# Optimization experiments

Hardware: AMD Instinct MI355X
Metric: run time of the kernel (lower is better)

## Reference

```python
import jax, jax.numpy as jnp
import numpy as np

DIM, HID, NC = 512, 102, 64
B, NS, ND, M = 256, 196, 196, 40
EPS_LN = 1e-5


def setup_inputs() -> dict:
    key = jax.random.key(0)
    ks = jax.random.split(key, 8)
    s = lambda d: 1.0 / np.sqrt(d)
    return {
        "tokens_sparse": jax.random.normal(ks[0], (B, NS, DIM), jnp.float32),
        "tokens_dense": jax.random.normal(ks[1], (B, ND, DIM), jnp.float32),
        "words": jax.random.normal(ks[2], (B, M, DIM), jnp.float32),
        "ln_g_s": jnp.ones((DIM,), jnp.float32),
        "ln_b_s": jnp.zeros((DIM,), jnp.float32),
        "w1_s": jax.random.normal(ks[3], (DIM, HID), jnp.float32) * s(DIM),
        "b1_s": jnp.zeros((HID,), jnp.float32),
        "w2_s": jax.random.normal(ks[4], (HID, NC), jnp.float32) * s(HID),
        "b2_s": jnp.zeros((NC,), jnp.float32),
        "ln_g_d": jnp.ones((DIM,), jnp.float32),
        "ln_b_d": jnp.zeros((DIM,), jnp.float32),
        "w1_d": jax.random.normal(ks[5], (DIM, HID), jnp.float32) * s(DIM),
        "b1_d": jnp.zeros((HID,), jnp.float32),
        "w2_d": jax.random.normal(ks[6], (HID, NC), jnp.float32) * s(HID),
        "b2_d": jnp.zeros((NC,), jnp.float32),
        "scale": jnp.ones((1, 1, 1), jnp.float32),
    }


def _layernorm(x, g, b):
    mu = x.mean(-1, keepdims=True)
    var = ((x - mu) ** 2).mean(-1, keepdims=True)
    return (x - mu) * jax.lax.rsqrt(var + EPS_LN) * g + b


def _aggregate(x, ln_g, ln_b, w1, b1, w2, b2, scale):
    # weight = MLP(LN(x)) -> (B, N, NC); transpose -> (B, NC, N); softmax over N; bmm
    h = jax.nn.gelu(_layernorm(x, ln_g, ln_b) @ w1 + b1, approximate=False)
    w = jnp.swapaxes(h @ w2 + b2, 1, 2) * scale            # (B, NC, N)
    w = jax.nn.softmax(w, axis=2)
    return jnp.einsum("bkn,bnc->bkc", w, x)                 # (B, NC, C)


def _l2norm(x):
    return x / jnp.maximum(jnp.linalg.norm(x, axis=-1, keepdims=True), 1e-8)


def reference(tokens_sparse, tokens_dense, words,
              ln_g_s, ln_b_s, w1_s, b1_s, w2_s, b2_s,
              ln_g_d, ln_b_d, w1_d, b1_d, w2_d, b2_d, scale):
    # DualTokenAggregation: paper Eq.(4)
    agg = _aggregate(tokens_sparse, ln_g_s, ln_b_s, w1_s, b1_s, w2_s, b2_s, scale)
    agg = agg + _aggregate(tokens_dense, ln_g_d, ln_b_d, w1_d, b1_d, w2_d, b2_d, scale)
    v = _l2norm(agg)                                        # (B, NC, C)
    t = _l2norm(words)                                      # (B, M, C)
    # HRPA (scan=True, bidirectional, no mask): bmm + leaky_relu + max/mean pooling
    sim = jnp.einsum("bmc,bkc->bmk", t, v)                  # (B, M, NC)
    sim = jnp.where(sim >= 0, sim, 0.1 * sim)               # leaky_relu(0.1)
    row_mean = sim.max(axis=2).mean(axis=1, keepdims=True)  # word->patch
    col_mean = sim.max(axis=1).mean(axis=1, keepdims=True)  # patch->word
    return row_mean + col_mean                              # (B, 1)
```

## Files before the change

### kernel.cpp

```cpp
#include <hip/hip_runtime.h>
#include <hip/hip_fp16.h>
#include <math.h>

#define Bb 256
#define Nn 196
#define Dd 512
#define Hh 102
#define Kk 64
#define Mm 40

#define LOGITS_BYTES 25690112
#define W1H_OFF  ((size_t)25690112)
#define W1L_OFF  (W1H_OFF + 262144)
#define GWB1_OFF (W1L_OFF + 262144)
#define W2TH_OFF (GWB1_OFF + 2048)
#define W2TL_OFF (W2TH_OFF + 32768)
#define H_OFF    (W2TL_OFF + 32768)
#define HL_OFF   (H_OFF + 29360128)
#define AGG_OFF  (HL_OFF + 29360128)

using short8 = __attribute__((ext_vector_type(8))) short;
using f32x4  = __attribute__((ext_vector_type(4))) float;

__device__ __forceinline__ void barrier_lgkm_only() {
  asm volatile("s_waitcnt lgkmcnt(0)" ::: "memory");
  __builtin_amdgcn_s_barrier();
  asm volatile("" ::: "memory");
}

__device__ __forceinline__ float dot4(const float4 a, const float4 b) {
  return a.x*b.x + a.y*b.y + a.z*b.z + a.w*b.w;
}
__device__ __forceinline__ float4 ld4s(const float* p) { return *(const float4*)p; }
__device__ __forceinline__ float gelu1(float z) {
  return 0.5f * z * (1.f + erff(z * 0.70710678118f));
}
__device__ __forceinline__ unsigned short bf16hi(float v) {
  return (unsigned short)(__float_as_uint(v) >> 16);
}
__device__ __forceinline__ float hipart(float v) {
  return __uint_as_float(__float_as_uint(v) & 0xffff0000u);
}
__device__ __forceinline__ unsigned short f2h(float v) {
  __half h = __float2half(v);
  return *(unsigned short*)&h;
}
__device__ __forceinline__ float h2f(unsigned short u) {
  __half h = *(__half*)&u;
  return __half2float(h);
}
__device__ __forceinline__ void split8(const float4 va, const float4 vb,
                                       short8& hh, short8& ll) {
  hh[0] = (short)bf16hi(va.x); ll[0] = (short)bf16hi(va.x - hipart(va.x));
  hh[1] = (short)bf16hi(va.y); ll[1] = (short)bf16hi(va.y - hipart(va.y));
  hh[2] = (short)bf16hi(va.z); ll[2] = (short)bf16hi(va.z - hipart(va.z));
  hh[3] = (short)bf16hi(va.w); ll[3] = (short)bf16hi(va.w - hipart(va.w));
  hh[4] = (short)bf16hi(vb.x); ll[4] = (short)bf16hi(vb.x - hipart(vb.x));
  hh[5] = (short)bf16hi(vb.y); ll[5] = (short)bf16hi(vb.y - hipart(vb.y));
  hh[6] = (short)bf16hi(vb.z); ll[6] = (short)bf16hi(vb.z - hipart(vb.z));
  hh[7] = (short)bf16hi(vb.w); ll[7] = (short)bf16hi(vb.w - hipart(vb.w));
}
__device__ __forceinline__ float wave_reduce_sum(float v) {
#pragma unroll
  for (int o = 1; o < 64; o <<= 1) v += __shfl_xor(v, o, 64);
  return v;
}
__device__ __forceinline__ float wave_reduce_max(float v) {
#pragma unroll
  for (int o = 1; o < 64; o <<= 1) v = fmaxf(v, __shfl_xor(v, o, 64));
  return v;
}

__global__ __launch_bounds__(512) void k0_wprep(
    const float* __restrict__ g_s, const float* __restrict__ b_s,
    const float* __restrict__ w1_s, const float* __restrict__ b1_s,
    const float* __restrict__ w2_s,
    const float* __restrict__ g_d, const float* __restrict__ b_d,
    const float* __restrict__ w1_d, const float* __restrict__ b1_d,
    const float* __restrict__ w2_d,
    unsigned short* __restrict__ w1h, unsigned short* __restrict__ w1l,
    float* __restrict__ gwb1,
    unsigned short* __restrict__ w2th, unsigned short* __restrict__ w2tl)
{
  const int p = blockIdx.x, slice = blockIdx.y;
  const float* g  = p ? g_d  : g_s;
  const float* bb = p ? b_d  : b_s;
  const float* w1 = p ? w1_d : w1_s;
  const float* b1 = p ? b1_d : b1_s;
  const float* w2 = p ? w2_d : w2_s;
  const int tid = threadIdx.x;

  if (slice < 8) {
    for (int idx = slice * 8192 + tid; idx < slice * 8192 + 8192; idx += 512) {
      const int j = idx & 127, c = idx >> 7;
      const float v = (j < Hh) ? w1[(size_t)c * Hh + j] * g[c] : 0.f;
      w1h[((size_t)(p * 128 + j)) * 512 + c] = bf16hi(v);
      w1l[((size_t)(p * 128 + j)) * 512 + c] = bf16hi(v - hipart(v));
    }
  } else {
    for (int idx = tid; idx < 8192; idx += 512) {
      const int k = idx >> 7, j = idx & 127;
      const float v = (j < Hh) ? w2[(size_t)j * Kk + k] : 0.f;
      w2th[(size_t)(p * 64 + k) * 128 + j] = bf16hi(v);
      w2tl[(size_t)(p * 64 + k) * 128 + j] = bf16hi(v - hipart(v));
    }
  }

  if (slice == 0) {
    __shared__ float red[4][128][2];
    const int j = tid & 127, part = tid >> 7;
    float sg = 0.f, sb = 0.f;
    if (j < Hh) {
      for (int c = part * 128; c < part * 128 + 128; ++c) {
        const float w = w1[(size_t)c * Hh + j];
        sg += g[c] * w;
        sb += bb[c] * w;
      }
    }
    red[part][j][0] = sg;
    red[part][j][1] = sb;
    __syncthreads();
    if (part == 0) {
      const float G  = red[0][j][0] + red[1][j][0] + red[2][j][0] + red[3][j][0];
      const float Bv = red[0][j][1] + red[1][j][1] + red[2][j][1] + red[3][j][1];
      gwb1[(p * 128 + j) * 2]     = G;
      gwb1[(p * 128 + j) * 2 + 1] = (j < Hh) ? (Bv + b1[j]) : 0.f;
    }
  }
}

__global__ __launch_bounds__(512) void k1a_hgemm(
    const float* __restrict__ x_s, const float* __restrict__ x_d,
    const unsigned short* __restrict__ w1h, const unsigned short* __restrict__ w1l,
    const float* __restrict__ gwb1,
    unsigned short* __restrict__ h_hi, unsigned short* __restrict__ h_lo)
{
  __shared__ __align__(16) char smem1[40320];
  unsigned short* xbuf = (unsigned short*)smem1;
  float* part = (float*)(smem1 + 35840);
  float* st   = (float*)(smem1 + 39424);

  const int tid = threadIdx.x;
  const int ntile = blockIdx.x, p = blockIdx.y, b = blockIdx.z;
  const int nbase = ntile * 112;
  const float* x  = p ? x_d : x_s;

  const int lane = tid & 63, wv = tid >> 6;
  const int lr = lane & 15, lg = lane >> 4;
  const int jb = wv * 16;
  const unsigned short* wph = w1h + ((size_t)(p * 128 + jb + lr)) * 512 + lg * 8;
  const unsigned short* wpl = w1l + ((size_t)(p * 128 + jb + lr)) * 512 + lg * 8;

  const int t = tid >> 2, q = tid & 3;
  const bool stg = (tid < 448);
  const int n = nbase + t;
  const bool valid = stg && (n < Nn);
  const float* xrow = x + ((size_t)(b * Nn + (valid ? n : 0))) * Dd + q * 8;

  float psum = 0.f, psq = 0.f;
  f32x4 acc0 = {0,0,0,0}, acc1 = acc0, acc2 = acc0, acc3 = acc0;
  f32x4 acc4 = acc0, acc5 = acc0, acc6 = acc0;

  short8 bh_c = *(const short8*)(wph);
  short8 bl_c = *(const short8*)(wpl);

  {
    float4 va = {0,0,0,0}, vb = va;
    if (valid) { va = ld4s(xrow); vb = ld4s(xrow + 4); }
    if (stg) {
      psum += va.x + va.y + va.z + va.w + vb.x + vb.y + vb.z + vb.w;
      psq  += dot4(va, va) + dot4(vb, vb);
      short8 hh, ll;
      split8(va, vb, hh, ll);
      *(short8*)(xbuf + t * 40 + q * 8) = hh;
      *(short8*)(xbuf + 4480 + t * 40 + q * 8) = ll;
    }
  }
  float4 pva = {0,0,0,0}, pvb = pva;
  if (valid) { pva = ld4s(xrow + 32); pvb = ld4s(xrow + 36); }
  barrier_lgkm_only();

#pragma unroll 1
  for (int ch = 0; ch < 16; ++ch) {
    const int buf = ch & 1;
    const unsigned short* xh = xbuf + buf * 8960;
    const unsigned short* xl = xh + 4480;

    float4 nva = {0,0,0,0}, nvb = nva;
    if (ch < 14 && valid) {
      const int co = (ch + 2) * 32;
      nva = ld4s(xrow + co);
      nvb = ld4s(xrow + co + 4);
    }
    short8 bh_n = bh_c, bl_n = bl_c;
    if (ch < 15) {
      const int co = (ch + 1) * 32;
      bh_n = *(const short8*)(wph + co);
      bl_n = *(const short8*)(wpl + co);
    }

#define MSTEP(A, M) { \
    const short8 ah = *(const short8*)(xh + ((M) * 16 + lr) * 40 + lg * 8); \
    const short8 al = *(const short8*)(xl + ((M) * 16 + lr) * 40 + lg * 8); \
    (A) = __builtin_amdgcn_mfma_f32_16x16x32_bf16(ah, bh_c, (A), 0, 0, 0); \
    (A) = __builtin_amdgcn_mfma_f32_16x16x32_bf16(ah, bl_c, (A), 0, 0, 0); \
    (A) = __builtin_amdgcn_mfma_f32_16x16x32_bf16(al, bh_c, (A), 0, 0, 0); }
    MSTEP(acc0, 0) MSTEP(acc1, 1) MSTEP(acc2, 2) MSTEP(acc3, 3)
    MSTEP(acc4, 4) MSTEP(acc5, 5) MSTEP(acc6, 6)
#undef MSTEP

    if (ch < 15 && stg) {
      psum += pva.x + pva.y + pva.z + pva.w + pvb.x + pvb.y + pvb.z + pvb.w;
      psq  += dot4(pva, pva) + dot4(pvb, pvb);
      short8 hh, ll;
      split8(pva, pvb, hh, ll);
      unsigned short* xw = xbuf + (buf ^ 1) * 8960;
      *(short8*)(xw + t * 40 + q * 8) = hh;
      *(short8*)(xw + 4480 + t * 40 + q * 8) = ll;
    }
    pva = nva; pvb = nvb;
    bh_c = bh_n; bl_c = bl_n;
    barrier_lgkm_only();
  }

  if (stg) {
    part[t * 8 + q * 2]     = psum;
    part[t * 8 + q * 2 + 1] = psq;
  }
  __syncthreads();
  if (tid < 112) {
    const float s  = part[tid * 8] + part[tid * 8 + 2] + part[tid * 8 + 4] + part[tid * 8 + 6];
    const float ss = part[tid * 8 + 1] + part[tid * 8 + 3] + part[tid * 8 + 5] + part[tid * 8 + 7];
    const float mu  = s * (1.f / 512.f);
    const float var = fmaxf(ss * (1.f / 512.f) - mu * mu, 0.f);
    st[2 * tid]     = mu;
    st[2 * tid + 1] = rsqrtf(var + 1e-5f);
  }
  __syncthreads();

  const int colw = jb + lr;
  const float Gw = gwb1[(p * 128 + colw) * 2];
  const float B1 = gwb1[(p * 128 + colw) * 2 + 1];
  const size_t hoff = (size_t)((b * 2 + p) * 2 + ntile) * 14336 + colw;
#define HW1(A, M) { \
    _Pragma("unroll") \
    for (int rr = 0; rr < 4; ++rr) { \
      const int row = (M) * 16 + lg * 4 + rr; \
      const float mu = st[2 * row], rs = st[2 * row + 1]; \
      const float hv = gelu1(rs * (A)[rr] - mu * rs * Gw + B1); \
      h_hi[hoff + row * 128] = bf16hi(hv); \
      h_lo[hoff + row * 128] = bf16hi(hv - hipart(hv)); \
    } }
  HW1(acc0, 0) HW1(acc1, 1) HW1(acc2, 2) HW1(acc3, 3)
  HW1(acc4, 4) HW1(acc5, 5) HW1(acc6, 6)
#undef HW1
}

__global__ __launch_bounds__(448) void k1b_logits(
    const unsigned short* __restrict__ h_hi, const unsigned short* __restrict__ h_lo,
    const unsigned short* __restrict__ w2th, const unsigned short* __restrict__ w2tl,
    const float* __restrict__ b2_s, const float* __restrict__ b2_d,
    float* __restrict__ logits)
{
  const int tid = threadIdx.x;
  const int ntile = blockIdx.x, p = blockIdx.y, b = blockIdx.z;
  const int nbase = ntile * 112;
  const float* b2 = p ? b2_d : b2_s;

  const int lane = tid & 63, wv = tid >> 6;
  const int lr = lane & 15, lg = lane >> 4;
  const size_t hbase = (size_t)((b * 2 + p) * 2 + ntile) * 14336;
  const unsigned short* hh = h_hi + hbase + (wv * 16 + lr) * 128 + lg * 8;
  const unsigned short* hl = h_lo + hbase + (wv * 16 + lr) * 128 + lg * 8;
  const unsigned short* w2hb = w2th + (size_t)p * 8192 + lr * 128 + lg * 8;
  const unsigned short* w2lb = w2tl + (size_t)p * 8192 + lr * 128 + lg * 8;

  f32x4 C0 = {0,0,0,0}, C1 = C0, C2 = C0, C3 = C0;

#define P2STEP(JG) { \
    const short8 Ah = *(const short8*)(hh + (JG)); \
    const short8 Al = *(const short8*)(hl + (JG)); \
    const short8 Bh0 = *(const short8*)(w2hb + (JG)); \
    const short8 Bl0 = *(const short8*)(w2lb + (JG)); \
    const short8 Bh1 = *(const short8*)(w2hb + 16 * 128 + (JG)); \
    const short8 Bl1 = *(const short8*)(w2lb + 16 * 128 + (JG)); \
    const short8 Bh2 = *(const short8*)(w2hb + 32 * 128 + (JG)); \
    const short8 Bl2 = *(const short8*)(w2lb + 32 * 128 + (JG)); \
    const short8 Bh3 = *(const short8*)(w2hb + 48 * 128 + (JG)); \
    const short8 Bl3 = *(const short8*)(w2lb + 48 * 128 + (JG)); \
    C0 = __builtin_amdgcn_mfma_f32_16x16x32_bf16(Ah, Bh0, C0, 0, 0, 0); \
    C0 = __builtin_amdgcn_mfma_f32_16x16x32_bf16(Ah, Bl0, C0, 0, 0, 0); \
    C0 = __builtin_amdgcn_mfma_f32_16x16x32_bf16(Al, Bh0, C0, 0, 0, 0); \
    C1 = __builtin_amdgcn_mfma_f32_16x16x32_bf16(Ah, Bh1, C1, 0, 0, 0); \
    C1 = __builtin_amdgcn_mfma_f32_16x16x32_bf16(Ah, Bl1, C1, 0, 0, 0); \
    C1 = __builtin_amdgcn_mfma_f32_16x16x32_bf16(Al, Bh1, C1, 0, 0, 0); \
    C2 = __builtin_amdgcn_mfma_f32_16x16x32_bf16(Ah, Bh2, C2, 0, 0, 0); \
    C2 = __builtin_amdgcn_mfma_f32_16x16x32_bf16(Ah, Bl2, C2, 0, 0, 0); \
    C2 = __builtin_amdgcn_mfma_f32_16x16x32_bf16(Al, Bh2, C2, 0, 0, 0); \
    C3 = __builtin_amdgcn_mfma_f32_16x16x32_bf16(Ah, Bh3, C3, 0, 0, 0); \
    C3 = __builtin_amdgcn_mfma_f32_16x16x32_bf16(Ah, Bl3, C3, 0, 0, 0); \
    C3 = __builtin_amdgcn_mfma_f32_16x16x32_bf16(Al, Bh3, C3, 0, 0, 0); }

  P2STEP(0) P2STEP(32) P2STEP(64) P2STEP(96)
#undef P2STEP

  const float bb0 = b2[lr], bb1 = b2[16 + lr];
  const float bb2 = b2[32 + lr], bb3 = b2[48 + lr];
#pragma unroll
  for (int rr = 0; rr < 4; ++rr) {
    const int tok = wv * 16 + lg * 4 + rr;
    const int nn = nbase + tok;
    if (nn < Nn) {
      float* lgp = logits + ((size_t)(b * 2 + p) * Nn + nn) * Kk;
      lgp[lr]      = C0[rr] + bb0;
      lgp[16 + lr] = C1[rr] + bb1;
      lgp[32 + lr] = C2[rr] + bb2;
      lgp[48 + lr] = C3[rr] + bb3;
    }
  }
}

__global__ __launch_bounds__(512) void k2_softmax_agg(
    const float* __restrict__ x_s, const float* __restrict__ x_d,
    const float* __restrict__ logits, const float* __restrict__ scale,
    unsigned short* __restrict__ aggP)
{
  __shared__ __align__(16) unsigned char smem2[68224];
  unsigned short* eh = (unsigned short*)smem2;
  unsigned short* el = (unsigned short*)(smem2 + 32768);
  float* rsk  = (float*)(smem2 + 65536);
  float* redf = (float*)(smem2 + 65792);
  float* mxk  = (float*)(smem2 + 67968);

  const int tid = threadIdx.x;
  const int p = blockIdx.x, b = blockIdx.y;
  const float sc = scale[0];
  const float* xb = (p ? x_d : x_s) + (size_t)b * Nn * Dd;

  const int kloc = tid & 63, sprt = tid >> 6;
  const float* lgp = logits + ((size_t)(b * 2 + p) * Nn) * Kk + kloc;
  const int eswz = (kloc & 31) << 3;
  float mx = -1e30f;
  for (int nn = sprt; nn < Nn; nn += 8) mx = fmaxf(mx, lgp[nn * 64] * sc);
  redf[sprt * 68 + kloc] = mx;
  __syncthreads();
  if (tid < 64) {
    float m = redf[tid];
#pragma unroll
    for (int gg = 1; gg < 8; ++gg) m = fmaxf(m, redf[gg * 68 + tid]);
    mxk[tid] = m;
  }
  __syncthreads();
  const float mk = mxk[kloc];
  float ssum = 0.f;
  for (int nn = sprt; nn < Nn; nn += 8) {
    const float e = expf(lgp[nn * 64] * sc - mk);
    const int ph = kloc * 256 + (nn ^ eswz);
    eh[ph] = bf16hi(e);
    el[ph] = bf16hi(e - hipart(e));
    ssum += e;
  }
  for (int nn = Nn + sprt; nn < 224; nn += 8) {
    const int ph = kloc * 256 + (nn ^ eswz);
    eh[ph] = 0; el[ph] = 0;
  }
  redf[sprt * 68 + kloc] = ssum;
  __syncthreads();
  if (tid < 64) {
    float s = 0.f;
#pragma unroll
    for (int gg = 0; gg < 8; ++gg) s += redf[gg * 68 + tid];
    rsk[tid] = 1.f / s;
  }
  __syncthreads();

  const int lane = tid & 63, wv = tid >> 6;
  const int lr = lane & 15, lg = lane >> 4;
  const int kt = wv & 3, ct = wv >> 2;
  const int arow = kt * 16 + lr;
  const int aswz = (arow & 31) << 3;
  const unsigned short* ebh = eh + arow * 256;
  const unsigned short* ebl = el + arow * 256;
  short8 Ah0, Ah1, Ah2, Ah3, Ah4, Ah5, Ah6;
  short8 Al0, Al1, Al2, Al3, Al4, Al5, Al6;
#define LDA(I) { const int off = ((I) * 32 + lg * 8) ^ aswz; \
  Ah##I = *(const short8*)(ebh + off); \
  Al##I = *(const short8*)(ebl + off); }
  LDA(0) LDA(1) LDA(2) LDA(3) LDA(4) LDA(5) LDA(6)
#undef LDA
  const int kbase = kt * 16 + lg * 4;
  const float r0 = rsk[kbase], r1 = rsk[kbase + 1];
  const float r2 = rsk[kbase + 2], r3 = rsk[kbase + 3];
  barrier_lgkm_only();

  const int brow = ct * 16 + lr;
  const int bswz = (brow & 31) << 3;
  const size_t agk = (size_t)((p * Bb + b) * Kk + kbase) * Dd;

#define K2STAGE(CHN, BUF) { \
    const int c0s = (CHN) * 32; \
    unsigned short* th = (unsigned short*)(smem2 + (BUF) * 32768); \
    unsigned short* tl = (unsigned short*)(smem2 + (BUF) * 32768 + 16384); \
    _Pragma("unroll") \
    for (int it = 0; it < 4; ++it) { \
      const int idx = it * 512 + tid; \
      const int cl = idx & 31, ngr = idx >> 5; \
      if (ngr < 56) { \
        const int n0 = ngr * 4; \
        const float* xpp = xb + (size_t)n0 * Dd + c0s + cl; \
        const float v0 = (n0     < Nn) ? xpp[0]      : 0.f; \
        const float v1 = (n0 + 1 < Nn) ? xpp[Dd]     : 0.f; \
        const float v2 = (n0 + 2 < Nn) ? xpp[2 * Dd] : 0.f; \
        const float v3 = (n0 + 3 < Nn) ? xpp[3 * Dd] : 0.f; \
        ushort4 hh4, ll4; \
        hh4.x = bf16hi(v0); ll4.x = bf16hi(v0 - hipart(v0)); \
        hh4.y = bf16hi(v1); ll4.y = bf16hi(v1 - hipart(v1)); \
        hh4.z = bf16hi(v2); ll4.z = bf16hi(v2 - hipart(v2)); \
        hh4.w = bf16hi(v3); ll4.w = bf16hi(v3 - hipart(v3)); \
        const int ph = cl * 256 + (n0 ^ ((cl & 31) << 3)); \
        *(ushort4*)(th + ph) = hh4; \
        *(ushort4*)(tl + ph) = ll4; \
      } \
    } }

  K2STAGE(0, 0)
  barrier_lgkm_only();

#pragma unroll 1
  for (int chn = 0; chn < 16; ++chn) {
    const int buf = chn & 1;
    if (chn < 15) { K2STAGE(chn + 1, buf ^ 1) }

    const unsigned short* bhb = (const unsigned short*)(smem2 + buf * 32768) + brow * 256;
    const unsigned short* blb = (const unsigned short*)(smem2 + buf * 32768 + 16384) + brow * 256;
    f32x4 acc = {0.f, 0.f, 0.f, 0.f};
#define K2KS(I) { \
    const int off = ((I) * 32 + lg * 8) ^ bswz; \
    const short8 Bh = *(const short8*)(bhb + off); \
    const short8 Bl = *(const short8*)(blb + off); \
    acc = __builtin_amdgcn_mfma_f32_16x16x32_bf16(Ah##I, Bh, acc, 0, 0, 0); \
    acc = __builtin_amdgcn_mfma_f32_16x16x32_bf16(Ah##I, Bl, acc, 0, 0, 0); \
    acc = __builtin_amdgcn_mfma_f32_16x16x32_bf16(Al##I, Bh, acc, 0, 0, 0); }
    K2KS(0) K2KS(1) K2KS(2) K2KS(3) K2KS(4) K2KS(5) K2KS(6)
#undef K2KS

    const int cc = chn * 32 + ct * 16 + lr;
    aggP[agk              + cc] = f2h(acc[0] * r0);
    aggP[agk +     (size_t)Dd + cc] = f2h(acc[1] * r1);
    aggP[agk + 2 * (size_t)Dd + cc] = f2h(acc[2] * r2);
    aggP[agk + 3 * (size_t)Dd + cc] = f2h(acc[3] * r3);
    barrier_lgkm_only();
  }
#undef K2STAGE
}

__global__ __launch_bounds__(512) void k4_final(
    const float* __restrict__ words, const unsigned short* __restrict__ aggP,
    float* __restrict__ outp)
{
  __shared__ __align__(16) unsigned char vls[64 * 512];
  __shared__ float rowm[40];
  __shared__ float colp[8][72];
  const int tid = threadIdx.x, b = blockIdx.x;
  const int w = tid >> 6, lane = tid & 63;
  const unsigned short* a0 = aggP + (size_t)b * (Kk * Dd);
  const unsigned short* a1 = aggP + ((size_t)(Bb + b)) * (Kk * Dd);
  const float* wrd = words + (size_t)b * Mm * Dd;
  const int m0 = w * 5;

  float rnt0, rnt1, rnt2, rnt3, rnt4;
#define TNORM(R, I) { \
    const float* tr = wrd + (size_t)(m0 + (I)) * Dd + lane * 8; \
    float4 ta = ld4s(tr), tb = ld4s(tr + 4); \
    float ss = wave_reduce_sum(dot4(ta, ta) + dot4(tb, tb)); \
    R = 1.f / fmaxf(sqrtf(ss), 1e-8f); }
  TNORM(rnt0, 0) TNORM(rnt1, 1) TNORM(rnt2, 2) TNORM(rnt3, 3) TNORM(rnt4, 4)
#undef TNORM

  float acc0 = 0.f, acc1 = 0.f, acc2 = 0.f, acc3 = 0.f, acc4 = 0.f, vsq = 0.f;

#pragma unroll 1
  for (int chn = 0; chn < 4; ++chn) {
    const int c0 = chn * 128;
    __syncthreads();
#pragma unroll
    for (int s = 0; s < 2; ++s) {
      const int idx = tid + s * 512;
      const int k = idx >> 4, g2 = idx & 15;
      const unsigned short* ph0 = a0 + (size_t)k * Dd + c0 + g2 * 8;
      const unsigned short* ph1 = a1 + (size_t)k * Dd + c0 + g2 * 8;
      const ushort4 u0a = *(const ushort4*)(ph0);
      const ushort4 u0b = *(const ushort4*)(ph0 + 4);
      const ushort4 u1a = *(const ushort4*)(ph1);
      const ushort4 u1b = *(const ushort4*)(ph1 + 4);
      float4 sa = {h2f(u0a.x) + h2f(u1a.x), h2f(u0a.y) + h2f(u1a.y),
                   h2f(u0a.z) + h2f(u1a.z), h2f(u0a.w) + h2f(u1a.w)};
      float4 sb = {h2f(u0b.x) + h2f(u1b.x), h2f(u0b.y) + h2f(u1b.y),
                   h2f(u0b.z) + h2f(u1b.z), h2f(u0b.w) + h2f(u1b.w)};
      const int gc0 = g2 * 2, gc1 = gc0 + 1;
      *(float4*)(vls + k * 512 + ((gc0 ^ (k & 31)) << 4)) = sa;
      *(float4*)(vls + k * 512 + ((gc1 ^ (k & 31)) << 4)) = sb;
    }
    __syncthreads();
#pragma unroll 2
    for (int cc = 0; cc < 32; ++cc) {
      const float4 vv = *(const float4*)(vls + lane * 512 + ((cc ^ (lane & 31)) << 4));
      const float* tp = wrd + c0 + cc * 4;
      const float4 t0 = ld4s(tp + (size_t)(m0    ) * Dd);
      const float4 t1 = ld4s(tp + (size_t)(m0 + 1) * Dd);
      const float4 t2 = ld4s(tp + (size_t)(m0 + 2) * Dd);
      const float4 t3 = ld4s(tp + (size_t)(m0 + 3) * Dd);
      const float4 t4 = ld4s(tp + (size_t)(m0 + 4) * Dd);
      acc0 += dot4(t0, vv); acc1 += dot4(t1, vv); acc2 += dot4(t2, vv);
      acc3 += dot4(t3, vv); acc4 += dot4(t4, vv);
      vsq  += dot4(vv, vv);
    }
  }

  const float rnv = 1.f / fmaxf(sqrtf(vsq), 1e-8f);
  float cmax = -1e30f;
#define DOM(ACC, RNT, I) { \
    float s = (ACC) * (RNT) * rnv; \
    s = (s >= 0.f) ? s : 0.1f * s; \
    cmax = fmaxf(cmax, s); \
    float rm = wave_reduce_max(s); \
    if (lane == 0) rowm[m0 + (I)] = rm; }
  DOM(acc0, rnt0, 0) DOM(acc1, rnt1, 1) DOM(acc2, rnt2, 2)
  DOM(acc3, rnt3, 3) DOM(acc4, rnt4, 4)
#undef DOM
  colp[w][lane] = cmax;
  __syncthreads();
  if (w == 0) {
    float cm = colp[0][lane];
#pragma unroll
    for (int ww = 1; ww < 8; ++ww) cm = fmaxf(cm, colp[ww][lane]);
    const float csum = wave_reduce_sum(cm);
    const float rv = (lane < 40) ? rowm[lane] : 0.f;
    const float rsum = wave_reduce_sum(rv);
    if (lane == 0) outp[b] = rsum * (1.f / 40.f) + csum * (1.f / 64.f);
  }
}

extern "C" void kernel_launch(void* const* d_in, const int* in_sizes, int n_in,
                              void* d_out, int out_size, void* d_ws, size_t ws_size,
                              hipStream_t stream)
{
  const float* x_s   = (const float*)d_in[0];
  const float* x_d   = (const float*)d_in[1];
  const float* words = (const float*)d_in[2];
  const float* g_s   = (const float*)d_in[3];
  const float* b_s   = (const float*)d_in[4];
  const float* w1_s  = (const float*)d_in[5];
  const float* b1_s  = (const float*)d_in[6];
  const float* w2_s  = (const float*)d_in[7];
  const float* b2_s  = (const float*)d_in[8];
  const float* g_d   = (const float*)d_in[9];
  const float* b_d   = (const float*)d_in[10];
  const float* w1_d  = (const float*)d_in[11];
  const float* b1_d  = (const float*)d_in[12];
  const float* w2_d  = (const float*)d_in[13];
  const float* b2_d  = (const float*)d_in[14];
  const float* scale = (const float*)d_in[15];
  (void)in_sizes; (void)n_in; (void)out_size; (void)ws_size;

  char* ws = (char*)d_ws;
  float* logits        = (float*)ws;
  unsigned short* w1h  = (unsigned short*)(ws + W1H_OFF);
  unsigned short* w1l  = (unsigned short*)(ws + W1L_OFF);
  float* gwb1          = (float*)(ws + GWB1_OFF);
  unsigned short* w2th = (unsigned short*)(ws + W2TH_OFF);
  unsigned short* w2tl = (unsigned short*)(ws + W2TL_OFF);
  unsigned short* h_hi = (unsigned short*)(ws + H_OFF);
  unsigned short* h_lo = (unsigned short*)(ws + HL_OFF);
  unsigned short* aggP = (unsigned short*)(ws + AGG_OFF);

  hipLaunchKernelGGL(k0_wprep, dim3(2, 9), dim3(512), 0, stream,
                     g_s, b_s, w1_s, b1_s, w2_s, g_d, b_d, w1_d, b1_d, w2_d,
                     w1h, w1l, gwb1, w2th, w2tl);
  hipLaunchKernelGGL(k1a_hgemm, dim3(2, 2, 256), dim3(512), 0, stream,
                     x_s, x_d, w1h, w1l, gwb1, h_hi, h_lo);
  hipLaunchKernelGGL(k1b_logits, dim3(2, 2, 256), dim3(448), 0, stream,
                     h_hi, h_lo, w2th, w2tl, b2_s, b2_d, logits);
  hipLaunchKernelGGL(k2_softmax_agg, dim3(2, Bb), dim3(512), 0, stream,
                     x_s, x_d, logits, scale, aggP);
  hipLaunchKernelGGL(k4_final, dim3(256), dim3(512), 0, stream,
                     words, aggP, (float*)d_out);
}
```

Baseline: 294.2 us.

## Fuse logits GEMM into softmax-aggregate kernel, keep logits in shared memory

Removes the separate k1b_logits kernel and computes the h@w2 logits inside k2_softmax_agg with MFMA, storing them transposed in LDS (stride 233) rather than a 25MB global buffer. Softmax max/sum then read from LDS, and the bf16 hi/lo exp operands are built directly in registers by recomputing expf. This saves one launch and a global write plus read of the logits. In exchange each block does extra GEMM work before the aggregation and computes exp twice.

```diff
diff --git a/kernel.cpp b/kernel.cpp
--- a/kernel.cpp
+++ b/kernel.cpp
@@ -9,7 +9,6 @@
 #define Kk 64
 #define Mm 40
 
-#define LOGITS_BYTES 25690112
 #define W1H_OFF  ((size_t)25690112)
 #define W1L_OFF  (W1H_OFF + 262144)
 #define GWB1_OFF (W1L_OFF + 262144)
@@ -256,78 +255,15 @@
 #undef HW1
 }
 
-__global__ __launch_bounds__(448) void k1b_logits(
+__global__ __launch_bounds__(512) void k2_softmax_agg(
+    const float* __restrict__ x_s, const float* __restrict__ x_d,
     const unsigned short* __restrict__ h_hi, const unsigned short* __restrict__ h_lo,
     const unsigned short* __restrict__ w2th, const unsigned short* __restrict__ w2tl,
     const float* __restrict__ b2_s, const float* __restrict__ b2_d,
-    float* __restrict__ logits)
-{
-  const int tid = threadIdx.x;
-  const int ntile = blockIdx.x, p = blockIdx.y, b = blockIdx.z;
-  const int nbase = ntile * 112;
-  const float* b2 = p ? b2_d : b2_s;
-
-  const int lane = tid & 63, wv = tid >> 6;
-  const int lr = lane & 15, lg = lane >> 4;
-  const size_t hbase = (size_t)((b * 2 + p) * 2 + ntile) * 14336;
-  const unsigned short* hh = h_hi + hbase + (wv * 16 + lr) * 128 + lg * 8;
-  const unsigned short* hl = h_lo + hbase + (wv * 16 + lr) * 128 + lg * 8;
-  const unsigned short* w2hb = w2th + (size_t)p * 8192 + lr * 128 + lg * 8;
-  const unsigned short* w2lb = w2tl + (size_t)p * 8192 + lr * 128 + lg * 8;
-
-  f32x4 C0 = {0,0,0,0}, C1 = C0, C2 = C0, C3 = C0;
-
-#define P2STEP(JG) { \
-    const short8 Ah = *(const short8*)(hh + (JG)); \
-    const short8 Al = *(const short8*)(hl + (JG)); \
-    const short8 Bh0 = *(const short8*)(w2hb + (JG)); \
-    const short8 Bl0 = *(const short8*)(w2lb + (JG)); \
-    const short8 Bh1 = *(const short8*)(w2hb + 16 * 128 + (JG)); \
-    const short8 Bl1 = *(const short8*)(w2lb + 16 * 128 + (JG)); \
-    const short8 Bh2 = *(const short8*)(w2hb + 32 * 128 + (JG)); \
-    const short8 Bl2 = *(const short8*)(w2lb + 32 * 128 + (JG)); \
-    const short8 Bh3 = *(const short8*)(w2hb + 48 * 128 + (JG)); \
-    const short8 Bl3 = *(const short8*)(w2lb + 48 * 128 + (JG)); \
-    C0 = __builtin_amdgcn_mfma_f32_16x16x32_bf16(Ah, Bh0, C0, 0, 0, 0); \
-    C0 = __builtin_amdgcn_mfma_f32_16x16x32_bf16(Ah, Bl0, C0, 0, 0, 0); \
-    C0 = __builtin_amdgcn_mfma_f32_16x16x32_bf16(Al, Bh0, C0, 0, 0, 0); \
-    C1 = __builtin_amdgcn_mfma_f32_16x16x32_bf16(Ah, Bh1, C1, 0, 0, 0); \
-    C1 = __builtin_amdgcn_mfma_f32_16x16x32_bf16(Ah, Bl1, C1, 0, 0, 0); \
-    C1 = __builtin_amdgcn_mfma_f32_16x16x32_bf16(Al, Bh1, C1, 0, 0, 0); \
-    C2 = __builtin_amdgcn_mfma_f32_16x16x32_bf16(Ah, Bh2, C2, 0, 0, 0); \
-    C2 = __builtin_amdgcn_mfma_f32_16x16x32_bf16(Ah, Bl2, C2, 0, 0, 0); \
-    C2 = __builtin_amdgcn_mfma_f32_16x16x32_bf16(Al, Bh2, C2, 0, 0, 0); \
-    C3 = __builtin_amdgcn_mfma_f32_16x16x32_bf16(Ah, Bh3, C3, 0, 0, 0); \
-    C3 = __builtin_amdgcn_mfma_f32_16x16x32_bf16(Ah, Bl3, C3, 0, 0, 0); \
-    C3 = __builtin_amdgcn_mfma_f32_16x16x32_bf16(Al, Bh3, C3, 0, 0, 0); }
-
-  P2STEP(0) P2STEP(32) P2STEP(64) P2STEP(96)
-#undef P2STEP
-
-  const float bb0 = b2[lr], bb1 = b2[16 + lr];
-  const float bb2 = b2[32 + lr], bb3 = b2[48 + lr];
-#pragma unroll
-  for (int rr = 0; rr < 4; ++rr) {
-    const int tok = wv * 16 + lg * 4 + rr;
-    const int nn = nbase + tok;
-    if (nn < Nn) {
-      float* lgp = logits + ((size_t)(b * 2 + p) * Nn + nn) * Kk;
-      lgp[lr]      = C0[rr] + bb0;
-      lgp[16 + lr] = C1[rr] + bb1;
-      lgp[32 + lr] = C2[rr] + bb2;
-      lgp[48 + lr] = C3[rr] + bb3;
-    }
-  }
-}
-
-__global__ __launch_bounds__(512) void k2_softmax_agg(
-    const float* __restrict__ x_s, const float* __restrict__ x_d,
-    const float* __restrict__ logits, const float* __restrict__ scale,
-    unsigned short* __restrict__ aggP)
+    const float* __restrict__ scale, unsigned short* __restrict__ aggP)
 {
   __shared__ __align__(16) unsigned char smem2[68224];
-  unsigned short* eh = (unsigned short*)smem2;
-  unsigned short* el = (unsigned short*)(smem2 + 32768);
+  float* lgL  = (float*)smem2;
   float* rsk  = (float*)(smem2 + 65536);
   float* redf = (float*)(smem2 + 65792);
   float* mxk  = (float*)(smem2 + 67968);
@@ -336,12 +272,45 @@
   const int p = blockIdx.x, b = blockIdx.y;
   const float sc = scale[0];
   const float* xb = (p ? x_d : x_s) + (size_t)b * Nn * Dd;
+  const float* b2 = p ? b2_d : b2_s;
+
+  const int lane = tid & 63, wv = tid >> 6;
+  const int lr = lane & 15, lg = lane >> 4;
+
+  {
+    const int kt = wv & 3;
+    const unsigned short* awh = w2th + (size_t)p * 8192 + (kt * 16 + lr) * 128 + lg * 8;
+    const unsigned short* awl = w2tl + (size_t)p * 8192 + (kt * 16 + lr) * 128 + lg * 8;
+#pragma unroll 1
+    for (int i = 0; i < 7; ++i) {
+      const int nt = (wv >> 2) * 7 + i;
+      const int n = nt * 16 + lr;
+      const int tile = (n >= 112) ? 1 : 0;
+      const size_t hb = ((size_t)((b * 2 + p) * 2 + tile)) * 14336
+                      + (size_t)(n - tile * 112) * 128 + lg * 8;
+      f32x4 acc = {0.f, 0.f, 0.f, 0.f};
+#pragma unroll
+      for (int j0 = 0; j0 < 128; j0 += 32) {
+        const short8 Awh = *(const short8*)(awh + j0);
+        const short8 Awl = *(const short8*)(awl + j0);
+        const short8 Bh  = *(const short8*)(h_hi + hb + j0);
+        const short8 Bl  = *(const short8*)(h_lo + hb + j0);
+        acc = __builtin_amdgcn_mfma_f32_16x16x32_bf16(Awh, Bh, acc, 0, 0, 0);
+        acc = __builtin_amdgcn_mfma_f32_16x16x32_bf16(Awh, Bl, acc, 0, 0, 0);
+        acc = __builtin_amdgcn_mfma_f32_16x16x32_bf16(Awl, Bh, acc, 0, 0, 0);
+      }
+#pragma unroll
+      for (int rr = 0; rr < 4; ++rr) {
+        const int k = kt * 16 + lg * 4 + rr;
+        lgL[k * 233 + nt * 16 + lr] = acc[rr] + b2[k];
+      }
+    }
+  }
+  __syncthreads();
 
   const int kloc = tid & 63, sprt = tid >> 6;
-  const float* lgp = logits + ((size_t)(b * 2 + p) * Nn) * Kk + kloc;
-  const int eswz = (kloc & 31) << 3;
   float mx = -1e30f;
-  for (int nn = sprt; nn < Nn; nn += 8) mx = fmaxf(mx, lgp[nn * 64] * sc);
+  for (int nn = sprt; nn < Nn; nn += 8) mx = fmaxf(mx, lgL[kloc * 233 + nn] * sc);
   redf[sprt * 68 + kloc] = mx;
   __syncthreads();
   if (tid < 64) {
@@ -353,17 +322,7 @@
   __syncthreads();
   const float mk = mxk[kloc];
   float ssum = 0.f;
-  for (int nn = sprt; nn < Nn; nn += 8) {
-    const float e = expf(lgp[nn * 64] * sc - mk);
-    const int ph = kloc * 256 + (nn ^ eswz);
-    eh[ph] = bf16hi(e);
-    el[ph] = bf16hi(e - hipart(e));
-    ssum += e;
-  }
-  for (int nn = Nn + sprt; nn < 224; nn += 8) {
-    const int ph = kloc * 256 + (nn ^ eswz);
-    eh[ph] = 0; el[ph] = 0;
-  }
+  for (int nn = sprt; nn < Nn; nn += 8) ssum += expf(lgL[kloc * 233 + nn] * sc - mk);
   redf[sprt * 68 + kloc] = ssum;
   __syncthreads();
   if (tid < 64) {
@@ -374,20 +333,20 @@
   }
   __syncthreads();
 
-  const int lane = tid & 63, wv = tid >> 6;
-  const int lr = lane & 15, lg = lane >> 4;
   const int kt = wv & 3, ct = wv >> 2;
   const int arow = kt * 16 + lr;
-  const int aswz = (arow & 31) << 3;
-  const unsigned short* ebh = eh + arow * 256;
-  const unsigned short* ebl = el + arow * 256;
+  const float mka = mxk[arow];
   short8 Ah0, Ah1, Ah2, Ah3, Ah4, Ah5, Ah6;
   short8 Al0, Al1, Al2, Al3, Al4, Al5, Al6;
-#define LDA(I) { const int off = ((I) * 32 + lg * 8) ^ aswz; \
-  Ah##I = *(const short8*)(ebh + off); \
-  Al##I = *(const short8*)(ebl + off); }
-  LDA(0) LDA(1) LDA(2) LDA(3) LDA(4) LDA(5) LDA(6)
-#undef LDA
+#define BUILD(I) { short8 h8, l8; \
+  _Pragma("unroll") \
+  for (int e = 0; e < 8; ++e) { \
+    const int nA = (I) * 32 + lg * 8 + e; \
+    const float v = (nA < Nn) ? expf(lgL[arow * 233 + nA] * sc - mka) : 0.f; \
+    h8[e] = (short)bf16hi(v); l8[e] = (short)bf16hi(v - hipart(v)); } \
+  Ah##I = h8; Al##I = l8; }
+  BUILD(0) BUILD(1) BUILD(2) BUILD(3) BUILD(4) BUILD(5) BUILD(6)
+#undef BUILD
   const int kbase = kt * 16 + lg * 4;
   const float r0 = rsk[kbase], r1 = rsk[kbase + 1];
   const float r2 = rsk[kbase + 2], r3 = rsk[kbase + 3];
@@ -564,7 +523,6 @@
   (void)in_sizes; (void)n_in; (void)out_size; (void)ws_size;
 
   char* ws = (char*)d_ws;
-  float* logits        = (float*)ws;
   unsigned short* w1h  = (unsigned short*)(ws + W1H_OFF);
   unsigned short* w1l  = (unsigned short*)(ws + W1L_OFF);
   float* gwb1          = (float*)(ws + GWB1_OFF);
@@ -579,10 +537,8 @@
                      w1h, w1l, gwb1, w2th, w2tl);
   hipLaunchKernelGGL(k1a_hgemm, dim3(2, 2, 256), dim3(512), 0, stream,
                      x_s, x_d, w1h, w1l, gwb1, h_hi, h_lo);
-  hipLaunchKernelGGL(k1b_logits, dim3(2, 2, 256), dim3(448), 0, stream,
-                     h_hi, h_lo, w2th, w2tl, b2_s, b2_d, logits);
   hipLaunchKernelGGL(k2_softmax_agg, dim3(2, Bb), dim3(512), 0, stream,
-                     x_s, x_d, logits, scale, aggP);
+                     x_s, x_d, h_hi, h_lo, w2th, w2tl, b2_s, b2_d, scale, aggP);
   hipLaunchKernelGGL(k4_final, dim3(256), dim3(512), 0, stream,
                      words, aggP, (float*)d_out);
 }
```

Result: slower. 314.0 us (+6.7%).
